# Kernel tuning notes

Hardware: AMD Instinct MI355X
Metric: run time of the kernel (lower is better)

## Reference

```python
import jax, jax.numpy as jnp
import numpy as np

D_MODEL = 1024
NUM_HEADS = 8
KEY_DIM = 768      # int(1024*0.75)
VALUE_DIM = 1536   # int(1024*1.5)
HQK = KEY_DIM // NUM_HEADS    # 96
HV = VALUE_DIM // NUM_HEADS   # 192
D_CONV = 4
CHUNK = 64
B, L = 2, 4096


def silu(x):
    return x * jax.nn.sigmoid(x)


def causal_dwconv(x, w):
    # x: (B, L, C), w: (C, K) depthwise kernel; causal (left pad K-1), matches
    # torch Conv1d(padding=K-1) followed by [:, :L] slice.
    K = w.shape[1]
    Lx = x.shape[1]
    xp = jnp.pad(x, ((0, 0), (K - 1, 0), (0, 0)))
    out = xp[:, 0:Lx, :] * w[:, 0]
    for j in range(1, K):
        out = out + xp[:, j:j + Lx, :] * w[:, j]
    return out


def chunk_gated_delta_rule(q, k, v, beta, g, c):
    # q,k: (B,H,L,Dk) L2-normalized; v: (B,H,L,Dv); beta,g: (B,H,L)
    b, h, l, dk = q.shape
    dv = v.shape[-1]
    n = l // c  # L chosen as multiple of chunk size
    q = q * (dk ** -0.5)
    v = v * beta[..., None]
    kb = k * beta[..., None]
    rs = lambda x: x.reshape(b, h, n, c, x.shape[-1])
    q, k, v, kb = rs(q), rs(k), rs(v), rs(kb)
    dec = jnp.cumsum(g.reshape(b, h, n, c), axis=-1)        # (b,h,n,c)
    Lmask = jnp.exp(jnp.minimum(dec[..., :, None] - dec[..., None, :], 0.0))  # (b,h,n,c,c)
    tri_incl = jnp.triu(jnp.ones((c, c), bool))   # upper incl diag -> zeroed
    striu = jnp.triu(jnp.ones((c, c), bool), 1)   # strict upper
    I = jnp.eye(c, dtype=jnp.float32)
    KK = jnp.einsum('bhncd,bhnmd->bhncm', kb, k)  # k_beta @ k^T
    M1 = I + jnp.where(tri_incl, 0.0, KK * Lmask)
    M2 = I + jnp.where(tri_incl, 0.0, KK)
    Ib = jnp.broadcast_to(I, M1.shape)
    solve = lambda M: jax.lax.linalg.triangular_solve(
        M, Ib, left_side=True, lower=True, unit_diagonal=True)
    u_ = solve(M1) @ v       # k_cumsum (= u)
    kcd = solve(M2) @ kb     # k_cumdecay

    def step(S, xs):
        qi, ki, ui, kci, Lmi, di = xs
        ed = jnp.exp(di)[..., None]                 # (b,h,c,1)
        attn = jnp.where(striu, 0.0, jnp.einsum('bhcd,bhmd->bhcm', qi, ki) * Lmi)
        v_new = ui - jnp.einsum('bhcd,bhde->bhce', kci * ed, S)
        oi = jnp.einsum('bhcd,bhde->bhce', qi * ed, S) + attn @ v_new
        dl = di[..., -1]                            # (b,h)
        S = S * jnp.exp(dl)[..., None, None] + jnp.einsum(
            'bhcd,bhce->bhde', ki * jnp.exp(dl[..., None] - di)[..., None], v_new)
        return S, oi

    xs = tuple(jnp.moveaxis(t, 2, 0) for t in (q, k, u_, kcd, Lmask, dec))
    S0 = jnp.zeros((b, h, dk, dv), jnp.float32)
    _, o = jax.lax.scan(step, S0, xs)               # o: (n,b,h,c,dv)
    return jnp.moveaxis(o, 0, 2).reshape(b, h, l, dv)


def setup_inputs() -> dict:
    key = jax.random.key(0)
    ks = jax.random.split(key, 16)
    w = lambda k, shape: (jax.random.normal(k, shape, jnp.float32) * 0.02)
    dt = jnp.exp(jax.random.uniform(ks[10], (NUM_HEADS,)) *
                 (np.log(0.1) - np.log(0.001)) + np.log(0.001))
    dt = jnp.clip(dt, 0.0001, None)
    inv_dt = dt + jnp.log(-jnp.expm1(-dt))
    return {
        'u': jax.random.normal(ks[0], (B, L, D_MODEL), jnp.float32),
        'Wq': w(ks[1], (D_MODEL, KEY_DIM)),
        'Wk': w(ks[2], (D_MODEL, KEY_DIM)),
        'Wv': w(ks[3], (D_MODEL, VALUE_DIM)),
        'Wg': w(ks[4], (D_MODEL, VALUE_DIM)),
        'Wo': w(ks[5], (VALUE_DIM, D_MODEL)),
        'Wgk': w(ks[6], (D_MODEL, NUM_HEADS)),
        'Wb': w(ks[7], (D_MODEL, NUM_HEADS)),
        'b_b': jnp.zeros((NUM_HEADS,), jnp.float32),
        'A_log': jnp.log(jax.random.uniform(ks[8], (NUM_HEADS,), minval=0.001, maxval=16.0)),
        'dt_bias': inv_dt.astype(jnp.float32),
        'conv_q': w(ks[11], (KEY_DIM, D_CONV)) * 10.0,
        'conv_k': w(ks[12], (KEY_DIM, D_CONV)) * 10.0,
        'conv_v': w(ks[13], (VALUE_DIM, D_CONV)) * 10.0,
        'norm_w': jnp.ones((HV,), jnp.float32),
    }


def reference(u, Wq, Wk, Wv, Wg, Wo, Wgk, Wb, b_b, A_log, dt_bias,
              conv_q, conv_k, conv_v, norm_w):
    b, l, _ = u.shape
    q = silu(causal_dwconv(u @ Wq, conv_q))
    k = silu(causal_dwconv(u @ Wk, conv_k))
    v = silu(causal_dwconv(u @ Wv, conv_v))
    gk = u @ Wgk                                    # (B,L,H)
    gk = -jnp.exp(A_log) * jax.nn.softplus(gk + dt_bias)
    gk = gk.transpose(0, 2, 1)                      # (B,H,L)
    beta = jax.nn.sigmoid(u @ Wb + b_b).transpose(0, 2, 1)
    to_bhl = lambda x, d: x.reshape(b, l, NUM_HEADS, d).transpose(0, 2, 1, 3)
    q = to_bhl(q, HQK)
    k = to_bhl(k, HQK)
    v = to_bhl(v, HV)
    l2n = lambda x: x / jnp.maximum(jnp.linalg.norm(x, axis=-1, keepdims=True), 1e-12)
    q, k = l2n(q), l2n(k)
    o = chunk_gated_delta_rule(q, k, v, beta, gk, CHUNK)  # (B,H,L,HV)
    o = o.transpose(0, 2, 1, 3)                     # (B,L,H,HV)
    g = (u @ Wg).reshape(b, l, NUM_HEADS, HV)
    # RMSNormGated, norm_before_gate=True: norm(x)*weight*silu(g)
    on = o * jax.lax.rsqrt(jnp.mean(o * o, axis=-1, keepdims=True) + 1e-5) * norm_w
    on = on * silu(g)
    return on.reshape(b, l, VALUE_DIM) @ Wo
```

## Files before the change

kernel.cpp:

```cpp
#include <hip/hip_runtime.h>

using u16 = unsigned short;
using u32 = unsigned int;
typedef __bf16 bf16x8 __attribute__((ext_vector_type(8)));
typedef u16    u16x8  __attribute__((ext_vector_type(8)));
typedef float  f32x4  __attribute__((ext_vector_type(4)));
typedef float  f32x2  __attribute__((ext_vector_type(2)));
typedef u32    u32x4  __attribute__((ext_vector_type(4)));
typedef u32    u32x2  __attribute__((ext_vector_type(2)));

__device__ __forceinline__ float bf2f(u16 h){ u32 u = ((u32)h)<<16; float f; __builtin_memcpy(&f,&u,4); return f; }
__device__ __forceinline__ u16 f2bf(float f){ u32 u; __builtin_memcpy(&u,&f,4); u32 r = (u + 0x7FFFu + ((u>>16)&1u))>>16; return (u16)r; }
__device__ __forceinline__ float bflo(u32 w){ return bf2f((u16)(w & 0xFFFFu)); }
__device__ __forceinline__ float bfhiw(u32 w){ return bf2f((u16)(w >> 16)); }
__device__ __forceinline__ float sigx(float x){ float e = __expf(-fabsf(x)); float p = 1.f/(1.f+e); return (x>=0.f) ? p : 1.f-p; }

#define BAR_LGKM() asm volatile("s_waitcnt lgkmcnt(0)\n\ts_barrier" ::: "memory")

__device__ __forceinline__ float ldsc(const void* p, size_t i, bool f32){
  return f32 ? ((const float*)p)[i] : bf2f(((const u16*)p)[i]);
}
__device__ __forceinline__ u32x4 ld8bf(const void* p, size_t i, bool f32){
  if (!f32) return *(const u32x4*)((const u16*)p + i);
  const f32x4* q = (const f32x4*)((const float*)p + i);
  f32x4 a = q[0], b = q[1];
  u32x4 r;
  r.x = (u32)f2bf(a.x) | ((u32)f2bf(a.y)<<16);
  r.y = (u32)f2bf(a.z) | ((u32)f2bf(a.w)<<16);
  r.z = (u32)f2bf(b.x) | ((u32)f2bf(b.y)<<16);
  r.w = (u32)f2bf(b.z) | ((u32)f2bf(b.w)<<16);
  return r;
}
__device__ __forceinline__ void ld4w(const void* p, size_t i, bool f32,
                                     float& w0, float& w1, float& w2, float& w3){
  if (f32){ f32x4 v = *(const f32x4*)((const float*)p + i); w0=v.x; w1=v.y; w2=v.z; w3=v.w; }
  else { u32x2 v = *(const u32x2*)((const u16*)p + i); w0=bflo(v.x); w1=bfhiw(v.x); w2=bflo(v.y); w3=bfhiw(v.y); }
}


__global__ void detect_kernel(const u16* __restrict__ probe, int* __restrict__ flag){
  int t = threadIdx.x;
  int bad = 0;
  for (int i=t; i<1024; i+=64){
    u16 h = probe[i];
    int e = (h>>7)&0xFF;
    if (e >= 0xC0) bad = 1;
  }
  unsigned long long anyb = __ballot(bad);
  if (t==0) *flag = (anyb != 0ull) ? 1 : 0;
}

__global__ void transpose5(const void* __restrict__ Wq, const void* __restrict__ Wk,
                           const void* __restrict__ Wv, const void* __restrict__ Wg,
                           const void* __restrict__ Wo, const void* __restrict__ U,
                           u16* __restrict__ WqT, u16* __restrict__ WkT, u16* __restrict__ WvT,
                           u16* __restrict__ WgT, u16* __restrict__ WoT, u16* __restrict__ ubf,
                           const int* __restrict__ flagp){
  const bool f32 = (*flagp != 0);
  const int bid = blockIdx.x;
  const int t = threadIdx.x;
  if (bid >= 6144){
    size_t base = ((size_t)(bid-6144)*256 + t) * 16;
    u32x4 a = ld8bf(U, base, f32);
    u32x4 b = ld8bf(U, base+8, f32);
    *(u32x4*)(ubf + base)     = a;
    *(u32x4*)(ubf + base + 8) = b;
    return;
  }
  const void* in; u16* out; int C; int local;
  int R;
  if (bid < 768){ in=Wq; out=WqT; R=1024; C=768;  local=bid; }
  else if (bid < 1536){ in=Wk; out=WkT; R=1024; C=768;  local=bid-768; }
  else if (bid < 3072){ in=Wv; out=WvT; R=1024; C=1536; local=bid-1536; }
  else if (bid < 4608){ in=Wg; out=WgT; R=1024; C=1536; local=bid-3072; }
  else { in=Wo; out=WoT; R=1536; C=1024; local=bid-4608; }
  const int nCx = C>>5;
  const int c0 = (local % nCx)*32, r0 = (local / nCx)*32;
  __shared__ u16 tile[32][33];
  int tx = t & 31, ty = t >> 5;
  #pragma unroll
  for (int j=0;j<4;j++){
    int r = r0 + ty + j*8;
    size_t g = (size_t)r*C + c0 + tx;
    tile[ty+j*8][tx] = f32 ? f2bf(((const float*)in)[g]) : ((const u16*)in)[g];
  }
  __syncthreads();
  #pragma unroll
  for (int j=0;j<4;j++){ int c = c0 + ty + j*8; out[(size_t)c*R + r0 + tx] = tile[tx][ty+j*8]; }
}

__global__ __launch_bounds__(256,2) void gemm_bt(const void* __restrict__ A, const u16* __restrict__ Bt,
                                                 void* __restrict__ C, int M, int N, int K,
                                                 const int* __restrict__ flagp, int a_ext, int c_ext,
                                                 int sanitize){
  __shared__ __align__(16) u16 As[128*32];
  __shared__ __align__(16) u16 Bs[128*32];
  const int fl = *flagp;
  const bool af32 = a_ext && fl;
  const bool cf32 = c_ext && fl;
  const int t = threadIdx.x;
  const int bid = blockIdx.x;
  const int nbn = N>>7, rpx = (M>>7)>>3;
  const int x2 = bid & 7, s = bid >> 3;
  const int bm = (x2*rpx + s/nbn)*128;
  const int bn = (s % nbn)*128;
  const int wave = t>>6, lane = t&63, quad = lane>>4, l16 = lane&15;
  const int wm = (wave>>1)*64, wn = (wave&1)*64;
  f32x4 acc[4][4] = {};
  const int row0 = t>>2, kp = (t&3)*8;
  const size_t iA0 = (size_t)(bm+row0)*K + kp;
  const size_t iA1 = iA0 + (size_t)64*K;
  const u16* pB0 = Bt + (size_t)(bn+row0)*K + kp;
  const u16* pB1 = pB0 + (size_t)64*K;
  u32x4 ra0 = ld8bf(A, iA0, af32);
  u32x4 ra1 = ld8bf(A, iA1, af32);
  u32x4 rb0 = *(const u32x4*)pB0;
  u32x4 rb1 = *(const u32x4*)pB1;
  const int nk = K>>5;
  for (int kt=0; kt<nk; ++kt){
    __syncthreads();
    ((u32x4*)As)[t]     = ra0;
    ((u32x4*)As)[t+256] = ra1;
    ((u32x4*)Bs)[t]     = rb0;
    ((u32x4*)Bs)[t+256] = rb1;
    __syncthreads();
    if (kt+1 < nk){
      int o = (kt+1)*32;
      ra0 = ld8bf(A, iA0 + o, af32); ra1 = ld8bf(A, iA1 + o, af32);
      rb0 = *(const u32x4*)(pB0 + o); rb1 = *(const u32x4*)(pB1 + o);
    }
    bf16x8 af[4], bfv[4];
    #pragma unroll
    for (int i=0;i<4;i++){
      af[i]  = *(const bf16x8*)&As[(wm + i*16 + l16)*32 + quad*8];
      bfv[i] = *(const bf16x8*)&Bs[(wn + i*16 + l16)*32 + quad*8];
    }
    #pragma unroll
    for (int i=0;i<4;i++)
      #pragma unroll
      for (int j=0;j<4;j++)
        acc[i][j] = __builtin_amdgcn_mfma_f32_16x16x32_bf16(af[i], bfv[j], acc[i][j], 0,0,0);
  }
  #pragma unroll
  for (int i=0;i<4;i++)
    #pragma unroll
    for (int j=0;j<4;j++)
      #pragma unroll
      for (int r2=0;r2<4;r2++){
        int m = bm + wm + i*16 + quad*4 + r2;
        int n = bn + wn + j*16 + l16;
        float v = acc[i][j][r2];
        if (sanitize && !(v==v && v<1e30f && v>-1e30f)) v = 0.f;
        if (cf32) ((float*)C)[(size_t)m*N + n] = v;
        else      ((u16*)C)[(size_t)m*N + n] = f2bf(v);
      }
}

__global__ __launch_bounds__(256,2) void gemm_qkv(const u16* __restrict__ A,
                                                  const u16* __restrict__ BtQ, const u16* __restrict__ BtK,
                                                  const u16* __restrict__ BtV,
                                                  u16* __restrict__ Cq, u16* __restrict__ Ck, u16* __restrict__ Cv){
  __shared__ __align__(16) u16 As[128*32];
  __shared__ __align__(16) u16 Bs[128*32];
  const int t = threadIdx.x;
  const int bid = blockIdx.x;
  const int x2 = bid & 7, s = bid >> 3;
  const int bm = (x2*8 + s/24)*128;
  const int cgrp = s % 24;
  const u16* Bt; u16* C; int N, bn;
  if (cgrp < 6){ Bt=BtQ; C=Cq; N=768; bn=cgrp*128; }
  else if (cgrp < 12){ Bt=BtK; C=Ck; N=768; bn=(cgrp-6)*128; }
  else { Bt=BtV; C=Cv; N=1536; bn=(cgrp-12)*128; }
  const int K = 1024;
  const int wave = t>>6, lane = t&63, quad = lane>>4, l16 = lane&15;
  const int wm = (wave>>1)*64, wn = (wave&1)*64;
  f32x4 acc[4][4] = {};
  const int row0 = t>>2, kp = (t&3)*8;
  const u16* pA0 = A + (size_t)(bm+row0)*K + kp;
  const u16* pA1 = pA0 + (size_t)64*K;
  const u16* pB0 = Bt + (size_t)(bn+row0)*K + kp;
  const u16* pB1 = pB0 + (size_t)64*K;
  u32x4 ra0 = *(const u32x4*)pA0;
  u32x4 ra1 = *(const u32x4*)pA1;
  u32x4 rb0 = *(const u32x4*)pB0;
  u32x4 rb1 = *(const u32x4*)pB1;
  for (int kt=0; kt<32; ++kt){
    __syncthreads();
    ((u32x4*)As)[t]     = ra0;
    ((u32x4*)As)[t+256] = ra1;
    ((u32x4*)Bs)[t]     = rb0;
    ((u32x4*)Bs)[t+256] = rb1;
    __syncthreads();
    if (kt+1 < 32){
      int o = (kt+1)*32;
      ra0 = *(const u32x4*)(pA0 + o); ra1 = *(const u32x4*)(pA1 + o);
      rb0 = *(const u32x4*)(pB0 + o); rb1 = *(const u32x4*)(pB1 + o);
    }
    bf16x8 af[4], bfv[4];
    #pragma unroll
    for (int i=0;i<4;i++){
      af[i]  = *(const bf16x8*)&As[(wm + i*16 + l16)*32 + quad*8];
      bfv[i] = *(const bf16x8*)&Bs[(wn + i*16 + l16)*32 + quad*8];
    }
    #pragma unroll
    for (int i=0;i<4;i++)
      #pragma unroll
      for (int j=0;j<4;j++)
        acc[i][j] = __builtin_amdgcn_mfma_f32_16x16x32_bf16(af[i], bfv[j], acc[i][j], 0,0,0);
  }
  #pragma unroll
  for (int i=0;i<4;i++)
    #pragma unroll
    for (int j=0;j<4;j++)
      #pragma unroll
      for (int r2=0;r2<4;r2++){
        int m = bm + wm + i*16 + quad*4 + r2;
        int n = bn + wn + j*16 + l16;
        C[(size_t)m*N + n] = f2bf(acc[i][j][r2]);
      }
}

__global__ __launch_bounds__(256) void prep_kernel(
    const void* __restrict__ u, const void* __restrict__ Wgk, const void* __restrict__ Wb,
    const void* __restrict__ b_b, const void* __restrict__ A_log, const void* __restrict__ dt_b,
    const u16* __restrict__ qraw, const u16* __restrict__ kraw, const u16* __restrict__ vraw,
    const void* __restrict__ cq, const void* __restrict__ ck, const void* __restrict__ cv,
    float* __restrict__ gk, float* __restrict__ beta,
    u16* __restrict__ qn, u16* __restrict__ kn, u16* __restrict__ vb,
    const int* __restrict__ flagp){
  const bool f32 = (*flagp != 0);
  const int bl = blockIdx.x;
  const int b = bl>>12, l = bl&4095;
  const int t = threadIdx.x;
  __shared__ float s[768];
  __shared__ float red[4][16];
  __shared__ float nrm[8];
  __shared__ float bS2[8];

  {
    float accg[8] = {0,0,0,0,0,0,0,0};
    float accb[8] = {0,0,0,0,0,0,0,0};
    for (int d=t; d<1024; d+=256){
      float uv = ldsc(u, (size_t)bl*1024 + d, f32);
      u32x4 wg = ld8bf(Wgk, (size_t)d*8, f32);
      u32x4 wb = ld8bf(Wb,  (size_t)d*8, f32);
      accg[0] += uv*bflo(wg.x); accg[1] += uv*bfhiw(wg.x);
      accg[2] += uv*bflo(wg.y); accg[3] += uv*bfhiw(wg.y);
      accg[4] += uv*bflo(wg.z); accg[5] += uv*bfhiw(wg.z);
      accg[6] += uv*bflo(wg.w); accg[7] += uv*bfhiw(wg.w);
      accb[0] += uv*bflo(wb.x); accb[1] += uv*bfhiw(wb.x);
      accb[2] += uv*bflo(wb.y); accb[3] += uv*bfhiw(wb.y);
      accb[4] += uv*bflo(wb.z); accb[5] += uv*bfhiw(wb.z);
      accb[6] += uv*bflo(wb.w); accb[7] += uv*bfhiw(wb.w);
    }
    #pragma unroll
    for (int h=0;h<8;h++){
      #pragma unroll
      for (int off=32; off>=1; off>>=1){
        accg[h] += __shfl_down(accg[h], off);
        accb[h] += __shfl_down(accb[h], off);
      }
    }
    int wv = t>>6, lane = t&63;
    if (lane==0){
      #pragma unroll
      for (int h=0;h<8;h++){ red[wv][h]=accg[h]; red[wv][8+h]=accb[h]; }
    }
    __syncthreads();
    if (t<16){
      float sum = red[0][t]+red[1][t]+red[2][t]+red[3][t];
      if (t<8){
        int h=t;
        float x = sum + ldsc(dt_b, h, f32);
        float sp = (x>20.f) ? x : log1pf(__expf(x));
        gk[(size_t)(b*8+h)*4096 + l] = -__expf(ldsc(A_log, h, f32)) * sp;
      } else {
        int h=t-8;
        float x = sum + ldsc(b_b, h, f32);
        float bv = sigx(x);
        beta[(size_t)(b*8+h)*4096 + l] = bv;
        bS2[h] = bv;
      }
    }
  }
  __syncthreads();

  const int base = b*4096;
  for (int c=t; c<768; c+=256){
    float w0,w1,w2,w3; ld4w(cq, (size_t)c*4, f32, w0,w1,w2,w3);
    float acc = 0.f;
    if (l>=3) acc += bf2f(qraw[(size_t)(base+l-3)*768 + c])*w0;
    if (l>=2) acc += bf2f(qraw[(size_t)(base+l-2)*768 + c])*w1;
    if (l>=1) acc += bf2f(qraw[(size_t)(base+l-1)*768 + c])*w2;
    acc += bf2f(qraw[(size_t)(base+l)*768 + c])*w3;
    s[c] = acc*sigx(acc);
  }
  __syncthreads();
  {
    int h = t>>5, l32 = t&31;
    float p = 0.f;
    for (int i=l32; i<96; i+=32){ float x = s[h*96+i]; p += x*x; }
    p += __shfl_down(p,16,32); p += __shfl_down(p,8,32); p += __shfl_down(p,4,32);
    p += __shfl_down(p,2,32);  p += __shfl_down(p,1,32);
    if (l32==0) nrm[h] = fmaxf(sqrtf(p), 1e-12f);
  }
  __syncthreads();
  for (int c=t; c<768; c+=256){
    int hh = c/96; int d = c - hh*96;
    float v = s[c]/nrm[hh]*0.10206207261596575f;
    qn[((size_t)(b*8+hh)*4096 + l)*96 + d] = f2bf(v);
  }
  __syncthreads();
  for (int c=t; c<768; c+=256){
    float w0,w1,w2,w3; ld4w(ck, (size_t)c*4, f32, w0,w1,w2,w3);
    float acc = 0.f;
    if (l>=3) acc += bf2f(kraw[(size_t)(base+l-3)*768 + c])*w0;
    if (l>=2) acc += bf2f(kraw[(size_t)(base+l-2)*768 + c])*w1;
    if (l>=1) acc += bf2f(kraw[(size_t)(base+l-1)*768 + c])*w2;
    acc += bf2f(kraw[(size_t)(base+l)*768 + c])*w3;
    s[c] = acc*sigx(acc);
  }
  __syncthreads();
  {
    int h = t>>5, l32 = t&31;
    float p = 0.f;
    for (int i=l32; i<96; i+=32){ float x = s[h*96+i]; p += x*x; }
    p += __shfl_down(p,16,32); p += __shfl_down(p,8,32); p += __shfl_down(p,4,32);
    p += __shfl_down(p,2,32);  p += __shfl_down(p,1,32);
    if (l32==0) nrm[h] = fmaxf(sqrtf(p), 1e-12f);
  }
  __syncthreads();
  for (int c=t; c<768; c+=256){
    int hh = c/96; int d = c - hh*96;
    float v = s[c]/nrm[hh]*1.0f;
    kn[((size_t)(b*8+hh)*4096 + l)*96 + d] = f2bf(v);
  }
  for (int c=t; c<1536; c+=256){
    float w0,w1,w2,w3; ld4w(cv, (size_t)c*4, f32, w0,w1,w2,w3);
    float acc = 0.f;
    if (l>=3) acc += bf2f(vraw[(size_t)(base+l-3)*1536 + c])*w0;
    if (l>=2) acc += bf2f(vraw[(size_t)(base+l-2)*1536 + c])*w1;
    if (l>=1) acc += bf2f(vraw[(size_t)(base+l-1)*1536 + c])*w2;
    acc += bf2f(vraw[(size_t)(base+l)*1536 + c])*w3;
    int h = c/192; int d = c - h*192;
    vb[((size_t)(b*8+h)*4096 + l)*192 + d] = f2bf(acc*sigx(acc)*bS2[h]);
  }
}

__global__ __launch_bounds__(320,2) void chunkprep_kernel(
    const u16* __restrict__ qn, const u16* __restrict__ kn, const u16* __restrict__ vb,
    const float* __restrict__ beta, const float* __restrict__ gk,
    u16* __restrict__ attn, u16* __restrict__ kcd, u16* __restrict__ uA,
    float* __restrict__ edG, float* __restrict__ wG, float* __restrict__ aG){
  __shared__ __align__(16) u16 kS[64*104];
  __shared__ __align__(16) u16 qS[64*104];
  __shared__ float M1[64*64];
  __shared__ float M2[64*64];
  __shared__ float bS[64], dS[64];
  const int t = threadIdx.x;
  const int bhn = blockIdx.x;
  const size_t rowb = (size_t)bhn*64;
  const int w = t>>6, l = t&63, l16 = l&15, quad = l>>4;

  #pragma unroll
  for (int j=0;j<3;j++){
    int v = t + 320*j;
    if (v < 768){
      int rr = v/12, c8 = v - rr*12;
      size_t g = (rowb+rr)*96 + c8*8;
      *(u32x4*)&kS[rr*104 + c8*8] = *(const u32x4*)(kn + g);
      *(u32x4*)&qS[rr*104 + c8*8] = *(const u32x4*)(qn + g);
    }
  }
  if (t<64){
    bS[t] = beta[rowb+t];
    float g = gk[rowb+t];
    #pragma unroll
    for (int off=1; off<64; off<<=1){
      float xx = __shfl_up(g, off);
      if (t >= off) g += xx;
    }
    dS[t] = g;
    float dl = __shfl(g, 63);
    edG[rowb+t] = __expf(g);
    wG[rowb+t]  = __expf(dl - g);
    if (t==0) aG[bhn] = __expf(dl);
  }
  __syncthreads();

  float x[64];
  const int mode0 = (t<192) ? 0 : 1;
  const int c0 = (t<192) ? t : (t-192);
  const bool active = (t < 288);
  if (active){
    if (mode0==0){
      #pragma unroll
      for (int i=0;i<64;i++) x[i] = bf2f(vb[(rowb+i)*192 + c0]);
    } else {
      #pragma unroll
      for (int i=0;i<64;i++) x[i] = bS[i]*bf2f(kS[i*104 + c0]);
    }
  }

  if (t < 256){
    bf16x8 qA[3], kA[3];
    #pragma unroll
    for (int ks=0;ks<3;ks++){
      qA[ks] = *(const bf16x8*)&qS[(w*16+l16)*104 + ks*32 + quad*8];
      kA[ks] = *(const bf16x8*)&kS[(w*16+l16)*104 + ks*32 + quad*8];
    }
    const size_t ab = (size_t)bhn*4096;
    #pragma unroll
    for (int nt=0;nt<4;nt++){
      f32x4 aQ = {0.f,0.f,0.f,0.f}, aK = {0.f,0.f,0.f,0.f};
      #pragma unroll
      for (int ks=0;ks<3;ks++){
        bf16x8 Bf = *(const bf16x8*)&kS[(nt*16+l16)*104 + ks*32 + quad*8];
        aQ = __builtin_amdgcn_mfma_f32_16x16x32_bf16(qA[ks], Bf, aQ,0,0,0);
        aK = __builtin_amdgcn_mfma_f32_16x16x32_bf16(kA[ks], Bf, aK,0,0,0);
      }
      #pragma unroll
      for (int r=0;r<4;r++){
        int row = w*16 + quad*4 + r;
        int col = nt*16 + l16;
        float lm = __expf(fminf(dS[row]-dS[col], 0.f));
        attn[ab + row*64 + col] = (col<=row) ? f2bf(aQ[r]*lm) : (u16)0;
        if (col<row){
          float kkb = aK[r]*bS[row];
          M2[row*64+col] = kkb;
          M1[row*64+col] = kkb*lm;
        }
      }
    }
  }
  __syncthreads();

  if (active){
    const float* Mb = (mode0==0) ? M1 : M2;
    #pragma unroll
    for (int i=1;i<64;i++){
      float acc = x[i];
      #pragma unroll
      for (int m=0;m<i;m++) acc -= Mb[i*64+m]*x[m];
      x[i] = acc;
    }
    if (mode0==0){
      #pragma unroll
      for (int i=0;i<64;i++) uA[(rowb+i)*192 + c0] = f2bf(x[i]);
    } else {
      #pragma unroll
      for (int i=0;i<64;i++) kcd[(rowb+i)*96 + c0] = f2bf(x[i]);
    }
  }
}

__global__ __launch_bounds__(256,1) void scan_glin_kernel(
    const u16* __restrict__ qn, const u16* __restrict__ kn, const u16* __restrict__ kcd,
    const u16* __restrict__ attn, const u16* __restrict__ uA,
    const float* __restrict__ edG, const float* __restrict__ wG, const float* __restrict__ aG,
    u16* __restrict__ o,
    const u16* __restrict__ Ag, const u16* __restrict__ Btg,
    u16* __restrict__ Cg0, u16* __restrict__ Cg1, u16* __restrict__ Cg2, u16* __restrict__ Cg3){
  __shared__ __align__(16) char smem[33280];
  const int bid = blockIdx.x;
  const int t = threadIdx.x;

  if (bid >= 192){
    u16* As = (u16*)smem;
    u16* Bs = (u16*)(smem + 8192);
    const int j = bid - 192;
    const int x2 = j & 7, s = j >> 3;
    const int bm = (x2*8 + s/12)*128;
    const int bn = (s % 12)*128;
    const int wave = t>>6, lane = t&63, quad = lane>>4, l16 = lane&15;
    const int wm = (wave>>1)*64, wn = (wave&1)*64;
    f32x4 acc[4][4] = {};
    const int row0 = t>>2, kp = (t&3)*8;
    const u16* pA0 = Ag + (size_t)(bm+row0)*1024 + kp;
    const u16* pA1 = pA0 + (size_t)64*1024;
    const u16* pB0 = Btg + (size_t)(bn+row0)*1024 + kp;
    const u16* pB1 = pB0 + (size_t)64*1024;
    u32x4 ra0 = *(const u32x4*)pA0;
    u32x4 ra1 = *(const u32x4*)pA1;
    u32x4 rb0 = *(const u32x4*)pB0;
    u32x4 rb1 = *(const u32x4*)pB1;
    for (int kt=0; kt<32; ++kt){
      __syncthreads();
      ((u32x4*)As)[t]     = ra0;
      ((u32x4*)As)[t+256] = ra1;
      ((u32x4*)Bs)[t]     = rb0;
      ((u32x4*)Bs)[t+256] = rb1;
      __syncthreads();
      if (kt+1 < 32){
        int o2 = (kt+1)*32;
        ra0 = *(const u32x4*)(pA0 + o2); ra1 = *(const u32x4*)(pA1 + o2);
        rb0 = *(const u32x4*)(pB0 + o2); rb1 = *(const u32x4*)(pB1 + o2);
      }
      bf16x8 af[4], bfv[4];
      #pragma unroll
      for (int i=0;i<4;i++){
        af[i]  = *(const bf16x8*)&As[(wm + i*16 + l16)*32 + quad*8];
        bfv[i] = *(const bf16x8*)&Bs[(wn + i*16 + l16)*32 + quad*8];
      }
      #pragma unroll
      for (int i=0;i<4;i++)
        #pragma unroll
        for (int j2=0;j2<4;j2++)
          acc[i][j2] = __builtin_amdgcn_mfma_f32_16x16x32_bf16(af[i], bfv[j2], acc[i][j2], 0,0,0);
    }
    u16* Cp; int mo;
    if (bm < 5376){ Cp = Cg0; mo = bm; }
    else if (bm < 6656){ Cp = Cg1; mo = bm - 5376; }
    else if (bm < 7680){ Cp = Cg2; mo = bm - 6656; }
    else { Cp = Cg3; mo = bm - 7680; }
    #pragma unroll
    for (int i=0;i<4;i++)
      #pragma unroll
      for (int j2=0;j2<4;j2++)
        #pragma unroll
        for (int r2=0;r2<4;r2++){
          int m = mo + wm + i*16 + quad*4 + r2;
          int n = bn + wn + j2*16 + l16;
          Cp[(size_t)m*1536 + n] = f2bf(acc[i][j2][r2]);
        }
    return;
  }

  const int bh = bid % 16, eg = bid / 16;
  const int e0 = eg*16;
  const int w = t>>6, l = t&63, l16 = l&15, quad = l>>4;

  u16* kTS   = (u16*)smem;
  u16* vnewT = (u16*)(smem + 27648);
  u16* Sbf   = (u16*)(smem + 29952);

  for (int i=t; i<16*104; i+=256) Sbf[i] = 0;

  size_t rowb = (size_t)bh*4096;
  size_t ab   = (size_t)bh*64*4096;

  const int trS = t & 63, cqS = (t>>6)*24;
  u32x4 kreg[3];
  auto pfK = [&](size_t rowbN){
    const u16* src = kn + (rowbN + trS)*96 + cqS;
    #pragma unroll
    for (int j=0;j<3;j++) kreg[j] = *(const u32x4*)(src + j*8);
  };
  auto stKT = [&](int nb, float wgt){
    u16* dst = kTS + nb*6912;
    #pragma unroll
    for (int j=0;j<3;j++){
      const int d = cqS + j*8;
      u32x4 v = kreg[j];
      dst[(d+0)*72 + trS] = f2bf(bflo(v.x)*wgt);
      dst[(d+1)*72 + trS] = f2bf(bfhiw(v.x)*wgt);
      dst[(d+2)*72 + trS] = f2bf(bflo(v.y)*wgt);
      dst[(d+3)*72 + trS] = f2bf(bfhiw(v.y)*wgt);
      dst[(d+4)*72 + trS] = f2bf(bflo(v.z)*wgt);
      dst[(d+5)*72 + trS] = f2bf(bfhiw(v.z)*wgt);
      dst[(d+6)*72 + trS] = f2bf(bflo(v.w)*wgt);
      dst[(d+7)*72 + trS] = f2bf(bfhiw(v.w)*wgt);
    }
  };

  u32x4 kcdF[3], qF[3], attF[2]; u16 uF[4];
  auto pfAB = [&](size_t rowbN){
    #pragma unroll
    for (int ks=0; ks<3; ks++){
      size_t gg = (rowbN + w*16 + l16)*96 + ks*32 + quad*8;
      kcdF[ks] = *(const u32x4*)(kcd + gg);
      qF[ks]   = *(const u32x4*)(qn + gg);
    }
  };
  auto pfATT = [&](size_t abN){
    #pragma unroll
    for (int ks=0; ks<2; ks++)
      attF[ks] = *(const u32x4*)(attn + abN + (w*16 + l16)*64 + ks*32 + quad*8);
  };
  auto pfU = [&](size_t rowbN){
    #pragma unroll
    for (int r=0;r<4;r++)
      uF[r] = uA[(rowbN + w*16 + quad*4 + r)*192 + e0 + l16];
  };

  pfK(rowb);
  pfAB(rowb); pfU(rowb); pfATT(ab);
  f32x4 edC = *(const f32x4*)&edG[rowb + w*16 + quad*4];
  float wC = wG[rowb + trS];
  float aexpC = aG[rowb>>6];
  __syncthreads();
  stKT(0, wC);
  f32x4 Sreg[2] = {};

  for (int n=0;n<64;n++){
    const int b = n&1, nb = b^1;
    const size_t rowbN = rowb + 64;
    const size_t abN = ab + 4096;
    f32x4 edN = {0.f,0.f,0.f,0.f};
    float wN = 0.f, aexpN = 0.f;
    if (n<63){
      pfK(rowbN);
      edN = *(const f32x4*)&edG[rowbN + w*16 + quad*4];
      wN = wG[rowbN + trS];
      aexpN = aG[rowbN>>6];
    }
    f32x4 accA = {0.f,0.f,0.f,0.f}, accQ = {0.f,0.f,0.f,0.f};
    #pragma unroll
    for (int ks=0;ks<3;ks++){
      bf16x8 Bf = *(const bf16x8*)&Sbf[l16*104 + ks*32 + quad*8];
      accA = __builtin_amdgcn_mfma_f32_16x16x32_bf16(*(const bf16x8*)&kcdF[ks], Bf, accA,0,0,0);
      accQ = __builtin_amdgcn_mfma_f32_16x16x32_bf16(*(const bf16x8*)&qF[ks],  Bf, accQ,0,0,0);
    }
    #pragma unroll
    for (int r=0;r<4;r++){
      float vn = bf2f(uF[r]) - edC[r]*accA[r];
      vnewT[l16*72 + (w*16+quad*4+r)] = f2bf(vn);
      accQ[r] *= edC[r];
    }
    if (n<63){ pfAB(rowbN); pfU(rowbN); }
    BAR_LGKM();
    #pragma unroll
    for (int ks=0;ks<2;ks++){
      bf16x8 Bv = *(const bf16x8*)&vnewT[l16*72 + ks*32 + quad*8];
      accQ = __builtin_amdgcn_mfma_f32_16x16x32_bf16(*(const bf16x8*)&attF[ks], Bv, accQ,0,0,0);
    }
    #pragma unroll
    for (int r=0;r<4;r++)
      o[(rowb + w*16 + quad*4 + r)*192 + e0 + l16] = f2bf(accQ[r]);
    if (n<63) pfATT(abN);
    if (n<63) stKT(nb, wN);
    #pragma unroll
    for (int i=0;i<2;i++){
      int tid = w + 4*i;
      if (tid < 6){
        int mt = tid;
        f32x4 acc = (f32x4){0.f,0.f,0.f,0.f};
        #pragma unroll
        for (int ks=0;ks<2;ks++){
          bf16x8 ku = *(const bf16x8*)&kTS[b*6912 + (mt*16+l16)*72 + ks*32 + quad*8];
          bf16x8 Bv = *(const bf16x8*)&vnewT[l16*72 + ks*32 + quad*8];
          acc = __builtin_amdgcn_mfma_f32_16x16x32_bf16(ku, Bv, acc,0,0,0);
        }
        f32x4 ns;
        ns.x = Sreg[i].x*aexpC + acc.x;
        ns.y = Sreg[i].y*aexpC + acc.y;
        ns.z = Sreg[i].z*aexpC + acc.z;
        ns.w = Sreg[i].w*aexpC + acc.w;
        Sreg[i] = ns;
        u32x2 pv;
        pv.x = (u32)f2bf(ns.x) | ((u32)f2bf(ns.y)<<16);
        pv.y = (u32)f2bf(ns.z) | ((u32)f2bf(ns.w)<<16);
        *(u32x2*)&Sbf[l16*104 + mt*16 + quad*4] = pv;
      }
    }
    BAR_LGKM();
    rowb = rowbN; ab = abN;
    edC = edN; wC = wN; aexpC = aexpN;
  }
}

__global__ __launch_bounds__(192) void epilogue_kernel(const u16* __restrict__ o,
                                                       const u16* __restrict__ g0, const u16* __restrict__ g1,
                                                       const u16* __restrict__ g2, const u16* __restrict__ g3,
                                                       const void* __restrict__ nw, u16* __restrict__ on,
                                                       const int* __restrict__ flagp){
  const bool f32 = (*flagp != 0);
  const int bl = blockIdx.x; const int h = blockIdx.y; const int d = threadIdx.x;
  const int b = bl>>12, l = bl&4095;
  float x = bf2f(o[((size_t)(b*8+h)*4096 + l)*192 + d]);
  float p = x*x;
  p += __shfl_down(p,32); p += __shfl_down(p,16); p += __shfl_down(p,8);
  p += __shfl_down(p,4);  p += __shfl_down(p,2);  p += __shfl_down(p,1);
  __shared__ float red[3];
  int wv = d>>6;
  if ((d&63)==0) red[wv] = p;
  __syncthreads();
  float ss = red[0]+red[1]+red[2];
  float rs = rsqrtf(ss/192.f + 1e-5f);
  const u16* gp; int bo;
  if (bl < 5376){ gp = g0; bo = bl; }
  else if (bl < 6656){ gp = g1; bo = bl - 5376; }
  else if (bl < 7680){ gp = g2; bo = bl - 6656; }
  else { gp = g3; bo = bl - 7680; }
  float g = bf2f(gp[(size_t)bo*1536 + h*192 + d]);
  float val = x*rs*ldsc(nw, d, f32) * g*sigx(g);
  on[(size_t)bl*1536 + h*192 + d] = f2bf(val);
}

extern "C" void kernel_launch(void* const* d_in, const int* in_sizes, int n_in,
                              void* d_out, int out_size, void* d_ws, size_t ws_size,
                              hipStream_t stream){
  (void)in_sizes; (void)n_in; (void)out_size; (void)ws_size;
  const void* u     = d_in[0];
  const void* Wq    = d_in[1];
  const void* Wk    = d_in[2];
  const void* Wv    = d_in[3];
  const void* Wg    = d_in[4];
  const void* Wo    = d_in[5];
  const void* Wgk   = d_in[6];
  const void* Wb    = d_in[7];
  const void* b_b   = d_in[8];
  const void* A_log = d_in[9];
  const void* dt_b  = d_in[10];
  const void* cq    = d_in[11];
  const void* ck    = d_in[12];
  const void* cv    = d_in[13];
  const void* nw    = d_in[14];

  char* w = (char*)d_ws;
  size_t off = 0;
  auto take = [&](size_t bytes)->char*{
    char* p = w + off;
    off += (bytes + 255) & ~(size_t)255;
    return p;
  };
  int* flag = (int*)take(256);
  u16* WqT  = (u16*)take((size_t)768*1024*2);
  u16* WkT  = (u16*)take((size_t)768*1024*2);
  u16* WvT  = (u16*)take((size_t)1536*1024*2);
  u16* WgT  = (u16*)take((size_t)1536*1024*2);
  u16* WoT  = (u16*)take((size_t)1024*1536*2);
  u16* qraw = (u16*)take((size_t)8192*768*2);
  u16* kraw = (u16*)take((size_t)8192*768*2);
  u16* vraw = (u16*)take((size_t)8192*1536*2);
  u16* qn   = (u16*)take((size_t)8192*768*2);
  u16* kn   = (u16*)take((size_t)8192*768*2);
  u16* vb   = (u16*)take((size_t)8192*1536*2);
  u16* ubf  = (u16*)take((size_t)8192*1024*2);
  float* gkA   = (float*)WqT;
  float* betaA = gkA + 65536;
  float* edG   = betaA + 65536;
  float* wGA   = edG + 65536;
  float* aGA   = wGA + 65536;
  u16* attnA = qraw;
  u16* kcdA  = kraw;
  u16* uuA   = vraw;
  u16* oA    = vb;
  u16* onA   = vraw;
  u16* glin0 = (u16*)d_out;
  u16* glin1 = attnA + (size_t)1024*64*64;
  u16* glin2 = WvT;
  u16* glin3 = WkT;

  detect_kernel<<<1,64,0,stream>>>((const u16*)u, flag);
  transpose5<<<8192,256,0,stream>>>(Wq, Wk, Wv, Wg, Wo, u,
                                    WqT, WkT, WvT, WgT, WoT, ubf, flag);
  gemm_qkv<<<1536,256,0,stream>>>(ubf, WqT, WkT, WvT, qraw, kraw, vraw);
  prep_kernel<<<8192,256,0,stream>>>(u, Wgk, Wb, b_b, A_log, dt_b,
                                     qraw, kraw, vraw, cq, ck, cv,
                                     gkA, betaA, qn, kn, vb, flag);
  chunkprep_kernel<<<1024,320,0,stream>>>(qn, kn, vb, betaA, gkA, attnA, kcdA, uuA,
                                          edG, wGA, aGA);
  scan_glin_kernel<<<960,256,0,stream>>>(qn, kn, kcdA, attnA, uuA, edG, wGA, aGA, oA,
                                         ubf, WgT, glin0, glin1, glin2, glin3);
  epilogue_kernel<<<dim3(8192,8),192,0,stream>>>(oA, glin0, glin1, glin2, glin3, nw, onA, flag);
  gemm_bt<<<512,256,0,stream>>>(onA, WoT, d_out, 8192, 1024, 1536, flag, 0, 1, 1);
}
```

Measured before the change: 608.1 us.

## Precompute decay-weighted transposed K in chunkprep and load it directly into registers during scan

```diff
diff --git a/kernel.cpp b/kernel.cpp
--- a/kernel.cpp
+++ b/kernel.cpp
@@ -348,15 +348,15 @@
 }
 
 __global__ __launch_bounds__(320,2) void chunkprep_kernel(
-    const u16* __restrict__ qn, const u16* __restrict__ kn, const u16* __restrict__ vb,
+    const u16* __restrict__ qn, u16* __restrict__ knw, const u16* __restrict__ vb,
     const float* __restrict__ beta, const float* __restrict__ gk,
     u16* __restrict__ attn, u16* __restrict__ kcd, u16* __restrict__ uA,
-    float* __restrict__ edG, float* __restrict__ wG, float* __restrict__ aG){
+    float* __restrict__ edG, float* __restrict__ aG){
   __shared__ __align__(16) u16 kS[64*104];
   __shared__ __align__(16) u16 qS[64*104];
   __shared__ float M1[64*64];
   __shared__ float M2[64*64];
-  __shared__ float bS[64], dS[64];
+  __shared__ float bS[64], dS[64], wS2[64];
   const int t = threadIdx.x;
   const int bhn = blockIdx.x;
   const size_t rowb = (size_t)bhn*64;
@@ -368,7 +368,7 @@
     if (v < 768){
       int rr = v/12, c8 = v - rr*12;
       size_t g = (rowb+rr)*96 + c8*8;
-      *(u32x4*)&kS[rr*104 + c8*8] = *(const u32x4*)(kn + g);
+      *(u32x4*)&kS[rr*104 + c8*8] = *(const u32x4*)(knw + g);
       *(u32x4*)&qS[rr*104 + c8*8] = *(const u32x4*)(qn + g);
     }
   }
@@ -383,10 +383,15 @@
     dS[t] = g;
     float dl = __shfl(g, 63);
     edG[rowb+t] = __expf(g);
-    wG[rowb+t]  = __expf(dl - g);
+    wS2[t] = __expf(dl - g);
     if (t==0) aG[bhn] = __expf(dl);
   }
   __syncthreads();
+
+  for (int idx=t; idx<6144; idx+=320){
+    int d = idx>>6, ll = idx&63;
+    knw[(size_t)bhn*6144 + idx] = f2bf(bf2f(kS[ll*104 + d])*wS2[ll]);
+  }
 
   float x[64];
   const int mode0 = (t<192) ? 0 : 1;
@@ -455,13 +460,13 @@
 }
 
 __global__ __launch_bounds__(256,1) void scan_glin_kernel(
-    const u16* __restrict__ qn, const u16* __restrict__ kn, const u16* __restrict__ kcd,
+    const u16* __restrict__ qn, const u16* __restrict__ kTw, const u16* __restrict__ kcd,
     const u16* __restrict__ attn, const u16* __restrict__ uA,
-    const float* __restrict__ edG, const float* __restrict__ wG, const float* __restrict__ aG,
+    const float* __restrict__ edG, const float* __restrict__ aG,
     u16* __restrict__ o,
     const u16* __restrict__ Ag, const u16* __restrict__ Btg,
     u16* __restrict__ Cg0, u16* __restrict__ Cg1, u16* __restrict__ Cg2, u16* __restrict__ Cg3){
-  __shared__ __align__(16) char smem[33280];
+  __shared__ __align__(16) char smem[16640];
   const int bid = blockIdx.x;
   const int t = threadIdx.x;
 
@@ -526,44 +531,21 @@
     return;
   }
 
+  __builtin_amdgcn_s_setprio(1);
   const int bh = bid % 16, eg = bid / 16;
   const int e0 = eg*16;
   const int w = t>>6, l = t&63, l16 = l&15, quad = l>>4;
 
-  u16* kTS   = (u16*)smem;
-  u16* vnewT = (u16*)(smem + 27648);
-  u16* Sbf   = (u16*)(smem + 29952);
+  u16* vnewT = (u16*)smem;
+  u16* Sbf   = (u16*)(smem + 2304);
 
   for (int i=t; i<16*104; i+=256) Sbf[i] = 0;
 
   size_t rowb = (size_t)bh*4096;
   size_t ab   = (size_t)bh*64*4096;
 
-  const int trS = t & 63, cqS = (t>>6)*24;
-  u32x4 kreg[3];
-  auto pfK = [&](size_t rowbN){
-    const u16* src = kn + (rowbN + trS)*96 + cqS;
-    #pragma unroll
-    for (int j=0;j<3;j++) kreg[j] = *(const u32x4*)(src + j*8);
-  };
-  auto stKT = [&](int nb, float wgt){
-    u16* dst = kTS + nb*6912;
-    #pragma unroll
-    for (int j=0;j<3;j++){
-      const int d = cqS + j*8;
-      u32x4 v = kreg[j];
-      dst[(d+0)*72 + trS] = f2bf(bflo(v.x)*wgt);
-      dst[(d+1)*72 + trS] = f2bf(bfhiw(v.x)*wgt);
-      dst[(d+2)*72 + trS] = f2bf(bflo(v.y)*wgt);
-      dst[(d+3)*72 + trS] = f2bf(bfhiw(v.y)*wgt);
-      dst[(d+4)*72 + trS] = f2bf(bflo(v.z)*wgt);
-      dst[(d+5)*72 + trS] = f2bf(bfhiw(v.z)*wgt);
-      dst[(d+6)*72 + trS] = f2bf(bflo(v.w)*wgt);
-      dst[(d+7)*72 + trS] = f2bf(bfhiw(v.w)*wgt);
-    }
-  };
-
   u32x4 kcdF[3], qF[3], attF[2]; u16 uF[4];
+  u32x4 kuC[2][2], kuN[2][2];
   auto pfAB = [&](size_t rowbN){
     #pragma unroll
     for (int ks=0; ks<3; ks++){
@@ -582,26 +564,33 @@
     for (int r=0;r<4;r++)
       uF[r] = uA[(rowbN + w*16 + quad*4 + r)*192 + e0 + l16];
   };
-
-  pfK(rowb);
+  auto pfKU = [&](size_t chunkIdx, u32x4 (&dst)[2][2]){
+    #pragma unroll
+    for (int i=0;i<2;i++){
+      int tid = w + 4*i;
+      if (tid < 6){
+        size_t base = chunkIdx*6144 + (size_t)(tid*16 + l16)*64 + quad*8;
+        dst[i][0] = *(const u32x4*)(kTw + base);
+        dst[i][1] = *(const u32x4*)(kTw + base + 32);
+      }
+    }
+  };
+
   pfAB(rowb); pfU(rowb); pfATT(ab);
+  pfKU(rowb>>6, kuC);
   f32x4 edC = *(const f32x4*)&edG[rowb + w*16 + quad*4];
-  float wC = wG[rowb + trS];
   float aexpC = aG[rowb>>6];
   __syncthreads();
-  stKT(0, wC);
   f32x4 Sreg[2] = {};
 
   for (int n=0;n<64;n++){
-    const int b = n&1, nb = b^1;
     const size_t rowbN = rowb + 64;
     const size_t abN = ab + 4096;
     f32x4 edN = {0.f,0.f,0.f,0.f};
-    float wN = 0.f, aexpN = 0.f;
+    float aexpN = 0.f;
     if (n<63){
-      pfK(rowbN);
+      pfKU(rowbN>>6, kuN);
       edN = *(const f32x4*)&edG[rowbN + w*16 + quad*4];
-      wN = wG[rowbN + trS];
       aexpN = aG[rowbN>>6];
     }
     f32x4 accA = {0.f,0.f,0.f,0.f}, accQ = {0.f,0.f,0.f,0.f};
@@ -628,7 +617,6 @@
     for (int r=0;r<4;r++)
       o[(rowb + w*16 + quad*4 + r)*192 + e0 + l16] = f2bf(accQ[r]);
     if (n<63) pfATT(abN);
-    if (n<63) stKT(nb, wN);
     #pragma unroll
     for (int i=0;i<2;i++){
       int tid = w + 4*i;
@@ -637,9 +625,8 @@
         f32x4 acc = (f32x4){0.f,0.f,0.f,0.f};
         #pragma unroll
         for (int ks=0;ks<2;ks++){
-          bf16x8 ku = *(const bf16x8*)&kTS[b*6912 + (mt*16+l16)*72 + ks*32 + quad*8];
           bf16x8 Bv = *(const bf16x8*)&vnewT[l16*72 + ks*32 + quad*8];
-          acc = __builtin_amdgcn_mfma_f32_16x16x32_bf16(ku, Bv, acc,0,0,0);
+          acc = __builtin_amdgcn_mfma_f32_16x16x32_bf16(*(const bf16x8*)&kuC[i][ks], Bv, acc,0,0,0);
         }
         f32x4 ns;
         ns.x = Sreg[i].x*aexpC + acc.x;
@@ -655,7 +642,8 @@
     }
     BAR_LGKM();
     rowb = rowbN; ab = abN;
-    edC = edN; wC = wN; aexpC = aexpN;
+    edC = edN; aexpC = aexpN;
+    kuC[0][0]=kuN[0][0]; kuC[0][1]=kuN[0][1]; kuC[1][0]=kuN[1][0]; kuC[1][1]=kuN[1][1];
   }
 }
 
@@ -750,8 +738,8 @@
                                      qraw, kraw, vraw, cq, ck, cv,
                                      gkA, betaA, qn, kn, vb, flag);
   chunkprep_kernel<<<1024,320,0,stream>>>(qn, kn, vb, betaA, gkA, attnA, kcdA, uuA,
-                                          edG, wGA, aGA);
-  scan_glin_kernel<<<960,256,0,stream>>>(qn, kn, kcdA, attnA, uuA, edG, wGA, aGA, oA,
+                                          edG, aGA);
+  scan_glin_kernel<<<960,256,0,stream>>>(qn, kn , kcdA, attnA, uuA, edG, aGA, oA,
                                          ubf, WgT, glin0, glin1, glin2, glin3);
   epilogue_kernel<<<dim3(8192,8),192,0,stream>>>(oA, glin0, glin1, glin2, glin3, nw, onA, flag);
   gemm_bt<<<512,256,0,stream>>>(onA, WoT, d_out, 8192, 1024, 1536, flag, 0, 1, 1);
```

Result: faster. 574.2 us (-5.6%).
